# Performance work log

Hardware: AMD Instinct MI355X
Metric: run time of the kernel (lower is better)

The kernel has to match this reference:

```python
import jax, jax.numpy as jnp
import numpy as np

RECALL_LO = 0.95
RECALL_HI = 1.0
LAMBDA_PAUC = 0.5
N = 8388608


def _pauc_binary(probs, t):
    # probs: [N] in (0,1), t: [N] float {0,1}
    order = jnp.argsort(-probs)                      # descending thresholds
    s = probs[order]
    pos = t[order]
    cp = jnp.cumsum(pos)                              # cumulative positives
    cn = jnp.cumsum(1.0 - pos)                        # cumulative negatives
    # Faithful to `probs >= threshold`: with ties, counts extend to the last
    # index sharing the same score. -s is ascending, so 'right' search gives
    # one past the last tie.
    r = jnp.searchsorted(-s, -s, side='right') - 1    # [N] last-tie index
    P = cp[-1]
    Ng = cn[-1]
    tpr = jnp.where(P > 0, cp[r] / P, 0.0)
    fpr = jnp.where(Ng > 0, cn[r] / Ng, 0.0)
    mask = (tpr >= RECALL_LO) & (tpr <= RECALL_HI)    # contiguous tail (tpr nondecreasing)
    y = jnp.clip(tpr - RECALL_LO, 0.0)
    pair = (mask[:-1] & mask[1:]).astype(probs.dtype)
    # trapezoid over the masked contiguous subsequence (== torch.trapz on the slice)
    return jnp.sum(pair * 0.5 * (y[:-1] + y[1:]) * (fpr[1:] - fpr[:-1]))


def _forward(predictions, targets):
    t = targets.astype(jnp.float32)                   # [N]
    logits = predictions[:, 0]                        # [N]
    # BCEWithLogitsLoss (mean reduction), numerically stable form
    ce = jnp.mean(jnp.maximum(logits, 0.0) - logits * t
                  + jnp.log1p(jnp.exp(-jnp.abs(logits))))
    probs = jax.nn.sigmoid(logits)
    pauc = _pauc_binary(probs, t)
    # binary path appends a single pauc value; weight = ones(2) -> sum = 2
    avg_pauc = pauc / (2.0 * (RECALL_HI - RECALL_LO))
    avg_pauc = jnp.clip(avg_pauc, 0.0, 1.0)
    pauc_loss = 1.0 - avg_pauc ** 2
    # torch.tensor(pauc) in the source detaches the pAUC branch from autograd
    pauc_loss = jax.lax.stop_gradient(pauc_loss)
    return (1.0 - LAMBDA_PAUC) * ce + LAMBDA_PAUC * pauc_loss


def setup_inputs() -> dict:
    key = jax.random.key(0)
    k1, k2 = jax.random.split(key)
    predictions = jax.random.normal(k1, (N, 1), dtype=jnp.float32)
    targets = jax.random.randint(k2, (N,), 0, 2, dtype=jnp.int32)
    return {"predictions": predictions, "targets": targets}


def reference(predictions, targets):
    return _forward(predictions, targets)
```

## Files before the change

kernel.cpp:

```cpp
#include <hip/hip_runtime.h>

#define HIST_BINS 1024
#define HIST_BYTES (HIST_BINS * 4)
#define KEY_SHIFT 22
#define NPART 16
#define RECALL_LO_C 0.95
#define GRID1 2048

__device__ __forceinline__ float softplus_neg(float a)
{
    const float LOG2E = 1.44269504088896341f;
    float t = fminf(a * LOG2E, 30.0f);
    float fi = rintf(t);
    float x = fi - t;
    float p = 1.535336188319500e-4f;
    p = p * x + 1.339887440266574e-3f;
    p = p * x + 9.618437357674640e-3f;
    p = p * x + 5.550332471162809e-2f;
    p = p * x + 2.402264791363012e-1f;
    p = p * x + 6.931472028550421e-1f;
    float m = p * x + 1.0f;
    int ii = (int)fi;
    float y = __uint_as_float(__float_as_uint(m) - ((unsigned int)ii << 23));
    float z1 = 1.0f + y;
    bool red = z1 > 1.41421356f;
    float zr = red ? z1 * 0.5f : z1;
    float el = red ? 0.69314718056f : 0.0f;
    float w  = zr - 1.0f;
    float zz = w * w;
    float q = 7.0376836292e-2f;
    q = q * w - 1.1514610310e-1f;
    q = q * w + 1.1676998740e-1f;
    q = q * w - 1.2420140846e-1f;
    q = q * w + 1.4249322787e-1f;
    q = q * w - 1.6668057665e-1f;
    q = q * w + 2.0000714765e-1f;
    q = q * w - 2.4999993993e-1f;
    q = q * w + 3.3333331174e-1f;
    return w + (w * zz * q - 0.5f * zz) + el;
}

__device__ __forceinline__ void process4(
    float4 x, int4 t, float& ce, unsigned int& pc, unsigned int* lhist)
{
    float xs[4] = {x.x, x.y, x.z, x.w};
    int   ts[4] = {t.x, t.y, t.z, t.w};
#pragma unroll
    for (int c = 0; c < 4; ++c) {
        float xv = xs[c];
        ce += fmaxf(xv, 0.0f) - xv * (float)ts[c] + softplus_neg(fabsf(xv));
        pc += (unsigned int)ts[c];
        unsigned int u = __float_as_uint(xv);
        int          m = (int)u >> 31;
        unsigned int key = u ^ (0x80000000u | (unsigned int)m);
        atomicAdd(&lhist[key >> KEY_SHIFT], ts[c] ? 65536u : 1u);
    }
}

__global__ __launch_bounds__(256) void pass1_kernel(
    const float* __restrict__ pred, const int* __restrict__ tgt,
    unsigned int* __restrict__ ghist, double* __restrict__ ce_part,
    unsigned int* __restrict__ pos_part, int n)
{
    __shared__ unsigned int lhist[HIST_BINS];

    uint4* lh4 = (uint4*)lhist;
    for (int b = threadIdx.x; b < HIST_BINS / 4; b += 256)
        lh4[b] = make_uint4(0u, 0u, 0u, 0u);
    __syncthreads();

    float ce = 0.0f;
    unsigned int pc = 0;

    const int tid    = blockIdx.x * blockDim.x + threadIdx.x;
    const int stride = gridDim.x * blockDim.x;
    const int n8     = n >> 3;

    const float4* p4 = (const float4*)pred;
    const int4*   t4 = (const int4*)tgt;

    for (int i = tid; i < n8; i += stride) {
        float4 x0 = p4[2 * i];
        float4 x1 = p4[2 * i + 1];
        int4   t0 = t4[2 * i];
        int4   t1 = t4[2 * i + 1];
        process4(x0, t0, ce, pc, lhist);
        process4(x1, t1, ce, pc, lhist);
    }
    for (int i = (n8 << 3) + tid; i < n; i += stride) {
        float xv = pred[i];
        int   ti = tgt[i];
        ce += fmaxf(xv, 0.0f) - xv * (float)ti + softplus_neg(fabsf(xv));
        pc += (unsigned int)ti;
        unsigned int u = __float_as_uint(xv);
        int          m = (int)u >> 31;
        unsigned int key = u ^ (0x80000000u | (unsigned int)m);
        atomicAdd(&lhist[key >> KEY_SHIFT], ti ? 65536u : 1u);
    }

    for (int off = 32; off > 0; off >>= 1) {
        ce += __shfl_down(ce, off);
        pc += __shfl_down(pc, off);
    }
    __shared__ float        lce[4];
    __shared__ unsigned int lpc[4];
    if ((threadIdx.x & 63) == 0) {
        lce[threadIdx.x >> 6] = ce;
        lpc[threadIdx.x >> 6] = pc;
    }
    __syncthreads();
    if (threadIdx.x == 0) {
        ce_part[blockIdx.x]  = (double)(lce[0] + lce[1] + lce[2] + lce[3]);
        pos_part[blockIdx.x] = lpc[0] + lpc[1] + lpc[2] + lpc[3];
    }

    const int nq  = HIST_BINS / 4;
    const int rot = (blockIdx.x * 16) & (nq - 1);
    unsigned int* gp = ghist + (blockIdx.x & (NPART - 1)) * HIST_BINS;
    {
        int b = ((int)threadIdx.x + rot) & (nq - 1);
        uint4 v = lh4[b];
        if (v.x) atomicAdd(&gp[4 * b + 0], v.x);
        if (v.y) atomicAdd(&gp[4 * b + 1], v.y);
        if (v.z) atomicAdd(&gp[4 * b + 2], v.z);
        if (v.w) atomicAdd(&gp[4 * b + 3], v.w);
    }
}

__global__ __launch_bounds__(256) void pass2_kernel(
    const unsigned int* __restrict__ hist, const double* __restrict__ ce_part,
    const unsigned int* __restrict__ pos_part, float* __restrict__ out, int n)
{
    __shared__ double sA[256];
    __shared__ double sB[256];

    const int tid = threadIdx.x;

    double ce_acc = 0.0, p_acc = 0.0;
    for (int i = tid; i < GRID1; i += 256) {
        ce_acc += ce_part[i];
        p_acc  += (double)pos_part[i];
    }
    sA[tid] = ce_acc;
    sB[tid] = p_acc;
    __syncthreads();
    for (int s = 128; s > 0; s >>= 1) {
        if (tid < s) { sA[tid] += sA[tid + s]; sB[tid] += sB[tid + s]; }
        __syncthreads();
    }
    const double CE_total = sA[0];
    const double Pd       = sB[0];
    __syncthreads();

    const int lo = HIST_BINS - (tid + 1) * 4;
    unsigned int pos[4] = {0,0,0,0};
    unsigned int neg[4] = {0,0,0,0};
    const uint4* h4 = (const uint4*)hist;
#pragma unroll
    for (int p = 0; p < NPART; ++p) {
        uint4 v = h4[p * (HIST_BINS / 4) + lo / 4];
        pos[0] += v.x >> 16;  neg[0] += v.x & 0xFFFFu;
        pos[1] += v.y >> 16;  neg[1] += v.y & 0xFFFFu;
        pos[2] += v.z >> 16;  neg[2] += v.z & 0xFFFFu;
        pos[3] += v.w >> 16;  neg[3] += v.w & 0xFFFFu;
    }

    double psum = (double)pos[0] + pos[1] + pos[2] + pos[3];
    sA[tid] = psum;
    __syncthreads();

    double v = psum;
    for (int s = 1; s < 256; s <<= 1) {
        double add = (tid >= s) ? sA[tid - s] : 0.0;
        __syncthreads();
        v += add;
        sA[tid] = v;
        __syncthreads();
    }
    double CP = v - psum;

    const double T = RECALL_LO_C * Pd;

    double S = 0.0;
#pragma unroll
    for (int i = 3; i >= 0; --i) {
        double p  = (double)pos[i];
        double ng = (double)neg[i];
        if (ng > 0.0) {
            double a = CP - T;
            double contrib;
            if (a >= 0.0) {
                contrib = a + 0.5 * p;
            } else {
                double ac = a + p;
                contrib = (ac > 0.0 && p > 0.0) ? (ac * ac) / (2.0 * p) : 0.0;
            }
            S += ng * contrib;
        }
        CP += p;
    }
    sB[tid] = S;
    __syncthreads();
    for (int s = 128; s > 0; s >>= 1) {
        if (tid < s) sB[tid] += sB[tid + s];
        __syncthreads();
    }

    if (tid == 0) {
        double Ng = (double)n - Pd;
        double pauc = 0.0;
        if (Pd > 0.0 && Ng > 0.0) pauc = sB[0] / (Pd * Ng);
        double avg = pauc / (2.0 * (1.0 - RECALL_LO_C));
        avg = fmin(fmax(avg, 0.0), 1.0);
        double ce = CE_total / (double)n;
        out[0] = (float)(0.5 * ce + 0.5 * (1.0 - avg * avg));
    }
}

extern "C" void kernel_launch(void* const* d_in, const int* in_sizes, int n_in,
                              void* d_out, int out_size, void* d_ws, size_t ws_size,
                              hipStream_t stream)
{
    const float* pred = (const float*)d_in[0];
    const int*   tgt  = (const int*)d_in[1];
    const int n = in_sizes[0];

    char* ws = (char*)d_ws;
    unsigned int* ghist    = (unsigned int*)ws;
    double*       ce_part  = (double*)(ws + NPART * HIST_BYTES);
    unsigned int* pos_part = (unsigned int*)(ws + NPART * HIST_BYTES + GRID1 * 8);

    hipMemsetAsync(d_ws, 0, NPART * HIST_BYTES, stream);

    pass1_kernel<<<GRID1, 256, 0, stream>>>(pred, tgt, ghist, ce_part, pos_part, n);
    pass2_kernel<<<1, 256, 0, stream>>>(ghist, ce_part, pos_part, (float*)d_out, n);
}
```

Before: 31.48 us.

## Use wave-contiguous 4x unrolled loads and double histogram partitions

Restructures the main loop so each wavefront reads four consecutive coalesced 64-lane float4 chunks of predictions and targets, giving more loads in flight per thread. It also doubles the number of global histogram partitions to reduce atomic contention when blocks flush their shared histograms. The cost is a larger memset, more partitions for the final kernel to sum, and higher register pressure from the extra outstanding loads.

```diff
diff --git a/kernel.cpp b/kernel.cpp
--- a/kernel.cpp
+++ b/kernel.cpp
@@ -3,7 +3,7 @@
 #define HIST_BINS 1024
 #define HIST_BYTES (HIST_BINS * 4)
 #define KEY_SHIFT 22
-#define NPART 16
+#define NPART 32
 #define RECALL_LO_C 0.95
 #define GRID1 2048
 
@@ -72,22 +72,40 @@
     float ce = 0.0f;
     unsigned int pc = 0;
 
-    const int tid    = blockIdx.x * blockDim.x + threadIdx.x;
-    const int stride = gridDim.x * blockDim.x;
-    const int n8     = n >> 3;
+    const int tid      = blockIdx.x * blockDim.x + threadIdx.x;
+    const int nthreads = gridDim.x * blockDim.x;
+    const int lane     = threadIdx.x & 63;
+    const int gwid     = tid >> 6;
+    const int nwaves   = nthreads >> 6;
+    const int n4       = n >> 2;
 
     const float4* p4 = (const float4*)pred;
     const int4*   t4 = (const int4*)tgt;
 
-    for (int i = tid; i < n8; i += stride) {
-        float4 x0 = p4[2 * i];
-        float4 x1 = p4[2 * i + 1];
-        int4   t0 = t4[2 * i];
-        int4   t1 = t4[2 * i + 1];
-        process4(x0, t0, ce, pc, lhist);
-        process4(x1, t1, ce, pc, lhist);
-    }
-    for (int i = (n8 << 3) + tid; i < n; i += stride) {
+    for (int wstart = gwid * 256; wstart < n4; wstart += nwaves * 256) {
+        if (wstart + 256 <= n4) {
+            float4 x0 = p4[wstart + 0 * 64 + lane];
+            float4 x1 = p4[wstart + 1 * 64 + lane];
+            float4 x2 = p4[wstart + 2 * 64 + lane];
+            float4 x3 = p4[wstart + 3 * 64 + lane];
+            int4   t0 = t4[wstart + 0 * 64 + lane];
+            int4   t1 = t4[wstart + 1 * 64 + lane];
+            int4   t2 = t4[wstart + 2 * 64 + lane];
+            int4   t3 = t4[wstart + 3 * 64 + lane];
+            process4(x0, t0, ce, pc, lhist);
+            process4(x1, t1, ce, pc, lhist);
+            process4(x2, t2, ce, pc, lhist);
+            process4(x3, t3, ce, pc, lhist);
+        } else {
+            for (int j = 0; j < 4; ++j) {
+                int idx = wstart + j * 64 + lane;
+                if (idx < n4) {
+                    process4(p4[idx], t4[idx], ce, pc, lhist);
+                }
+            }
+        }
+    }
+    for (int i = (n4 << 2) + tid; i < n; i += nthreads) {
         float xv = pred[i];
         int   ti = tgt[i];
         ce += fmaxf(xv, 0.0f) - xv * (float)ti + softplus_neg(fabsf(xv));
```

Result: faster. 30.46 us (-3.3%).
